# Kernel tuning notes

Hardware: AMD Instinct MI355X
Metric: run time of the kernel (lower is better)

The kernel has to match this reference:

```python
import jax, jax.numpy as jnp
import numpy as np

FEATURE_DIM = 256
NUM_HEADS = 8
HEAD_DIM = FEATURE_DIM // NUM_HEADS
LOCAL_RADIUS = 3.0
N_CUR = 4096
N_HIST = 4096
COORD_EXTENT = 16.0


def setup_inputs() -> dict:
    key = jax.random.key(0)
    ks = jax.random.split(key, 12)
    s = 1.0 / np.sqrt(FEATURE_DIM)  # ~nn.Linear init scale
    return {
        "current_feats": jax.random.normal(ks[0], (N_CUR, FEATURE_DIM), jnp.float32),
        "historical_feats": jax.random.normal(ks[1], (N_HIST, FEATURE_DIM), jnp.float32),
        "current_coords": jax.random.uniform(ks[2], (N_CUR, 3), jnp.float32) * COORD_EXTENT,
        "historical_coords": jax.random.uniform(ks[3], (N_HIST, 3), jnp.float32) * COORD_EXTENT,
        "Wq": jax.random.normal(ks[4], (FEATURE_DIM, FEATURE_DIM), jnp.float32) * s,
        "bq": jnp.zeros((FEATURE_DIM,), jnp.float32),
        "Wk": jax.random.normal(ks[5], (FEATURE_DIM, FEATURE_DIM), jnp.float32) * s,
        "bk": jnp.zeros((FEATURE_DIM,), jnp.float32),
        "Wv": jax.random.normal(ks[6], (FEATURE_DIM, FEATURE_DIM), jnp.float32) * s,
        "bv": jnp.zeros((FEATURE_DIM,), jnp.float32),
        "Wo": jax.random.normal(ks[7], (FEATURE_DIM, FEATURE_DIM), jnp.float32) * s,
        "bo": jnp.zeros((FEATURE_DIM,), jnp.float32),
    }


def reference(current_feats, historical_feats, current_coords, historical_coords,
              Wq, bq, Wk, bk, Wv, bv, Wo, bo):
    # local mask: squared distance <= radius^2 (identical to norm <= radius)
    diff = current_coords[:, None, :] - historical_coords[None, :, :]  # [Nq, Nk, 3]
    local_mask = jnp.sum(diff * diff, axis=-1) <= LOCAL_RADIUS ** 2      # [Nq, Nk]

    q = (current_feats @ Wq.T + bq).reshape(N_CUR, NUM_HEADS, HEAD_DIM)
    k = (historical_feats @ Wk.T + bk).reshape(N_HIST, NUM_HEADS, HEAD_DIM)
    v = (historical_feats @ Wv.T + bv).reshape(N_HIST, NUM_HEADS, HEAD_DIM)

    scores = jnp.einsum('qhd,khd->qhk', q, k) / np.sqrt(HEAD_DIM)        # [Nq, H, Nk]
    scores = jnp.where(local_mask[:, None, :], scores, -jnp.inf)
    attn = jax.nn.softmax(scores, axis=-1)  # dropout is identity in eval
    out = jnp.einsum('qhk,khd->qhd', attn, v).reshape(N_CUR, FEATURE_DIM)
    return out @ Wo.T + bo
```

## Files before the change

kernel.cpp:

```cpp
#include <hip/hip_runtime.h>
#include <math.h>

#define FDIM 256
#define NH 8
#define HD 32
#define NQ 4096
#define NKEY 4096
#define CAP 512
#define R2 9.0f

typedef _Float16 half8 __attribute__((ext_vector_type(8)));
typedef _Float16 half4v __attribute__((ext_vector_type(4)));
typedef float f32x4 __attribute__((ext_vector_type(4)));
typedef unsigned short ushort_t;

#define CB_CUR  0
#define CB_HIST 1048576
#define CB_WQ   2097152
#define CB_WK   2162688
#define CB_WV   2228224
#define CB_WO   2293760
#define CB_F4_TOTAL 589824

__global__ __launch_bounds__(256) void prep(const float* __restrict__ cur,
                                            const float* __restrict__ hist,
                                            const float* __restrict__ Wq,
                                            const float* __restrict__ Wk,
                                            const float* __restrict__ Wv,
                                            const float* __restrict__ Wo,
                                            _Float16* __restrict__ dst,
                                            const float* __restrict__ qc,
                                            const float* __restrict__ kc,
                                            ushort_t* __restrict__ nbr,
                                            int* __restrict__ cnt) {
    if (blockIdx.x < 1024) {
        const int q    = blockIdx.x * 4 + (threadIdx.x >> 6);
        const int lane = threadIdx.x & 63;
        const float qx = qc[q * 3 + 0];
        const float qy = qc[q * 3 + 1];
        const float qz = qc[q * 3 + 2];
        int base = 0;
        for (int k0 = 0; k0 < NKEY; k0 += 64) {
            const int k = k0 + lane;
            float dx = __fsub_rn(qx, kc[k * 3 + 0]);
            float dy = __fsub_rn(qy, kc[k * 3 + 1]);
            float dz = __fsub_rn(qz, kc[k * 3 + 2]);
            float d2 = __fadd_rn(__fadd_rn(__fmul_rn(dx, dx), __fmul_rn(dy, dy)),
                                 __fmul_rn(dz, dz));
            bool valid = (d2 <= R2);
            unsigned long long bal = __ballot(valid);
            if (valid) {
                int pos = base + __popcll(bal & ((1ull << lane) - 1ull));
                if (pos < CAP) nbr[(size_t)q * CAP + pos] = (ushort_t)k;
            }
            base += __popcll(bal);
        }
        if (lane == 0) cnt[q] = (base > CAP) ? CAP : base;
    } else {
        const int stride = 1024 * 256;
        for (int i4 = (blockIdx.x - 1024) * 256 + threadIdx.x; i4 < CB_F4_TOTAL;
             i4 += stride) {
            const float* src;
            int base;
            if (i4 < 262144)      { src = cur;  base = 0; }
            else if (i4 < 524288) { src = hist; base = 262144; }
            else if (i4 < 540672) { src = Wq;   base = 524288; }
            else if (i4 < 557056) { src = Wk;   base = 540672; }
            else if (i4 < 573440) { src = Wv;   base = 557056; }
            else                  { src = Wo;   base = 573440; }
            float4 v = ((const float4*)src)[i4 - base];
            half4v h;
            h[0] = (_Float16)v.x; h[1] = (_Float16)v.y;
            h[2] = (_Float16)v.z; h[3] = (_Float16)v.w;
            ((half4v*)dst)[i4] = h;
        }
    }
}

__device__ __forceinline__ void mfma_tile_16x64(const _Float16* __restrict__ A,
                                                const _Float16* __restrict__ W,
                                                int m0, int n0, int wave, int lane,
                                                f32x4 acc[4]) {
    const int row  = lane & 15;
    const int quad = lane >> 4;
    const _Float16* aptr = A + (size_t)(m0 + wave * 16 + row) * 256 + quad * 8;
    const _Float16* wptr = W + (size_t)(n0 + row) * 256 + quad * 8;
#pragma unroll
    for (int i = 0; i < 4; ++i) acc[i] = (f32x4){0.f, 0.f, 0.f, 0.f};
#pragma unroll
    for (int k0 = 0; k0 < 8; ++k0) {
        half8 a = *(const half8*)(aptr + k0 * 32);
#pragma unroll
        for (int nt = 0; nt < 4; ++nt) {
            half8 b = *(const half8*)(wptr + (size_t)nt * 16 * 256 + k0 * 32);
            acc[nt] = __builtin_amdgcn_mfma_f32_16x16x32_f16(a, b, acc[nt], 0, 0, 0);
        }
    }
}

__global__ __launch_bounds__(256) void qkv_mfma(const _Float16* __restrict__ cb,
                                                const float* __restrict__ bq,
                                                const float* __restrict__ bk,
                                                const float* __restrict__ bv,
                                                float* __restrict__ Qout,
                                                _Float16* __restrict__ KV) {
    const int z    = blockIdx.z;
    const int wave = threadIdx.x >> 6;
    const int lane = threadIdx.x & 63;
    const int m0   = blockIdx.y * 64;
    const int n0   = blockIdx.x * 64;

    const _Float16* A = (z == 0) ? (cb + CB_CUR) : (cb + CB_HIST);
    const _Float16* W = (z == 0) ? (cb + CB_WQ) : (z == 1) ? (cb + CB_WK) : (cb + CB_WV);
    const float* bias = (z == 0) ? bq : (z == 1) ? bk : bv;

    f32x4 acc[4];
    mfma_tile_16x64(A, W, m0, n0, wave, lane, acc);

    const int col  = lane & 15;
    const int quad = lane >> 4;
    float bs[4];
#pragma unroll
    for (int nt = 0; nt < 4; ++nt) bs[nt] = bias[n0 + nt * 16 + col];

    if (z == 0) {
#pragma unroll
        for (int nt = 0; nt < 4; ++nt)
#pragma unroll
            for (int r = 0; r < 4; ++r)
                Qout[(size_t)(m0 + wave * 16 + quad * 4 + r) * 256 + n0 + nt * 16 + col] =
                    acc[nt][r] + bs[nt];
    } else {
        const int off = (z == 1) ? 0 : 256;
#pragma unroll
        for (int nt = 0; nt < 4; ++nt)
#pragma unroll
            for (int r = 0; r < 4; ++r)
                KV[(size_t)(m0 + wave * 16 + quad * 4 + r) * 512 + off + n0 + nt * 16 + col] =
                    (_Float16)(acc[nt][r] + bs[nt]);
    }
}

__global__ __launch_bounds__(256) void o_mfma(const _Float16* __restrict__ Ob,
                                              const _Float16* __restrict__ Wo,
                                              const float* __restrict__ bo,
                                              float* __restrict__ out) {
    const int wave = threadIdx.x >> 6;
    const int lane = threadIdx.x & 63;
    const int m0   = blockIdx.y * 64;
    const int n0   = blockIdx.x * 64;

    f32x4 acc[4];
    mfma_tile_16x64(Ob, Wo, m0, n0, wave, lane, acc);

    const int col  = lane & 15;
    const int quad = lane >> 4;
#pragma unroll
    for (int nt = 0; nt < 4; ++nt) {
        const float b = bo[n0 + nt * 16 + col];
#pragma unroll
        for (int r = 0; r < 4; ++r)
            out[(size_t)(m0 + wave * 16 + quad * 4 + r) * 256 + n0 + nt * 16 + col] =
                acc[nt][r] + b;
    }
}

__global__ __launch_bounds__(256) void sparse_attn6(const float* __restrict__ Q,
                                                    const _Float16* __restrict__ KV,
                                                    const ushort_t* __restrict__ nbr,
                                                    const int* __restrict__ cnt,
                                                    _Float16* __restrict__ Ob) {
    __shared__ float sm[4][32][12];
    const int q    = blockIdx.x;
    const int t    = threadIdx.x;
    const int wave = t >> 6;
    const int lane = t & 63;
    const int p    = lane >> 5;
    const int h    = (lane >> 2) & 7;
    const int s    = lane & 3;

    float qv[8];
    {
        const float* qrow = Q + (size_t)q * FDIM + h * HD + s * 8;
        float4 a = ((const float4*)qrow)[0];
        float4 b = ((const float4*)qrow)[1];
        const float sc = 0.17677669529663687f;
        qv[0] = a.x * sc; qv[1] = a.y * sc; qv[2] = a.z * sc; qv[3] = a.w * sc;
        qv[4] = b.x * sc; qv[5] = b.y * sc; qv[6] = b.z * sc; qv[7] = b.w * sc;
    }

    float o[8];
#pragma unroll
    for (int i = 0; i < 8; ++i) o[i] = 0.f;
    float m = -3e38f, l = 0.f;

    const int n = cnt[q];
    const ushort_t* nl = nbr + (size_t)q * CAP;
    const int koff = h * HD + s * 8;

    for (int j = 2 * wave + p; j < n; j += 8) {
        const int k = nl[j];
        const _Float16* r = KV + ((size_t)k << 9) + koff;
        half8 k8 = *(const half8*)(r);
        half8 v8 = *(const half8*)(r + 256);

        float part = 0.f;
#pragma unroll
        for (int i = 0; i < 8; ++i)
            part = fmaf(qv[i], (float)k8[i], part);
        part += __shfl_xor(part, 1, 64);
        part += __shfl_xor(part, 2, 64);

        const float nm = fmaxf(m, part);
        const float sf = __expf(m - nm);
        const float pw = __expf(part - nm);
        l = l * sf + pw;
#pragma unroll
        for (int i = 0; i < 8; ++i)
            o[i] = o[i] * sf + pw * (float)v8[i];
        m = nm;
    }

    {
        const float m2 = __shfl_xor(m, 32, 64);
        const float l2 = __shfl_xor(l, 32, 64);
        const float nm = fmaxf(m, m2);
        const float a  = __expf(m - nm);
        const float b  = __expf(m2 - nm);
        l = l * a + l2 * b;
#pragma unroll
        for (int i = 0; i < 8; ++i) {
            const float o2 = __shfl_xor(o[i], 32, 64);
            o[i] = o[i] * a + o2 * b;
        }
        m = nm;
    }

    if (lane < 32) {
        float* dst = &sm[wave][lane][0];
        *(float4*)(dst)     = (float4){o[0], o[1], o[2], o[3]};
        *(float4*)(dst + 4) = (float4){o[4], o[5], o[6], o[7]};
        dst[8] = m; dst[9] = l;
    }
    __syncthreads();

    if (t < 32) {
        float4 x0 = *(const float4*)&sm[0][t][0];
        float4 x1 = *(const float4*)&sm[0][t][4];
        float O[8] = {x0.x, x0.y, x0.z, x0.w, x1.x, x1.y, x1.z, x1.w};
        float M = sm[0][t][8], L = sm[0][t][9];
#pragma unroll
        for (int w = 1; w < 4; ++w) {
            float4 y0 = *(const float4*)&sm[w][t][0];
            float4 y1 = *(const float4*)&sm[w][t][4];
            const float m2 = sm[w][t][8], l2 = sm[w][t][9];
            const float nm = fmaxf(M, m2);
            const float a  = __expf(M - nm);
            const float b  = __expf(m2 - nm);
            L = L * a + l2 * b;
            float y[8] = {y0.x, y0.y, y0.z, y0.w, y1.x, y1.y, y1.z, y1.w};
#pragma unroll
            for (int i = 0; i < 8; ++i) O[i] = O[i] * a + y[i] * b;
            M = nm;
        }
        const float inv = 1.0f / L;
        half8 ho;
#pragma unroll
        for (int i = 0; i < 8; ++i) ho[i] = (_Float16)(O[i] * inv);
        *(half8*)(Ob + (size_t)q * FDIM + t * 8) = ho;
    }
}

extern "C" void kernel_launch(void* const* d_in, const int* in_sizes, int n_in,
                              void* d_out, int out_size, void* d_ws, size_t ws_size,
                              hipStream_t stream) {
    const float* cur_feats   = (const float*)d_in[0];
    const float* hist_feats  = (const float*)d_in[1];
    const float* cur_coords  = (const float*)d_in[2];
    const float* hist_coords = (const float*)d_in[3];
    const float* bq = (const float*)d_in[5];
    const float* bk = (const float*)d_in[7];
    const float* bv = (const float*)d_in[9];
    const float* bo = (const float*)d_in[11];
    float* out = (float*)d_out;

    char* w = (char*)d_ws;
    float*     Qb   = (float*)(w);
    _Float16*  KV   = (_Float16*)(w + (4 << 20));
    ushort_t*  nbr  = (ushort_t*)(w + (8 << 20));
    int*       cnt  = (int*)(w + (12 << 20));
    _Float16*  Ob   = (_Float16*)(w + (12 << 20) + (64 << 10));
    _Float16*  cb   = (_Float16*)(w + (15 << 20));

    prep<<<2048, 256, 0, stream>>>(cur_feats, hist_feats,
                                   (const float*)d_in[4], (const float*)d_in[6],
                                   (const float*)d_in[8], (const float*)d_in[10], cb,
                                   cur_coords, hist_coords, nbr, cnt);

    qkv_mfma<<<dim3(4, 64, 3), 256, 0, stream>>>(cb, bq, bk, bv, Qb, KV);

    sparse_attn6<<<NQ, 256, 0, stream>>>(Qb, KV, nbr, cnt, Ob);

    o_mfma<<<dim3(4, 64), 256, 0, stream>>>(Ob, cb + CB_WO, bo, out);
}
```

Baseline: 150.1 us.

## Group spatially nearby queries per block to share K/V neighbor loads

Queries are binned into a 6x6x6 spatial grid, and each attention block handles up to four queries from the same cell. The block builds a shared union of their neighbor lists with per-query masks, so each K/V row is loaded once and used for all four queries. Q is also stored in fp16 to halve its traffic. In exchange the block pays bitmap and union-list construction with atomics and extra syncs, and does masked softmax work on keys outside a query's own radius.

After: 230.7 us. 53.7% more time.

```diff
diff --git a/kernel.cpp b/kernel.cpp
--- a/kernel.cpp
+++ b/kernel.cpp
@@ -8,6 +8,14 @@
 #define NKEY 4096
 #define CAP 512
 #define R2 9.0f
+
+#define NCELL 6
+#define NC3   216
+#define CCAP  64
+#define NGRP  16
+#define GBLK  (NC3 * NGRP)
+#define OCAP  512
+#define OBLK  64
 
 typedef _Float16 half8 __attribute__((ext_vector_type(8)));
 typedef _Float16 half4v __attribute__((ext_vector_type(4)));
@@ -32,7 +40,11 @@
                                             const float* __restrict__ qc,
                                             const float* __restrict__ kc,
                                             ushort_t* __restrict__ nbr,
-                                            int* __restrict__ cnt) {
+                                            int* __restrict__ cnt,
+                                            int* __restrict__ ccnt,
+                                            int* __restrict__ cellq,
+                                            int* __restrict__ ocnt,
+                                            int* __restrict__ oq) {
     if (blockIdx.x < 1024) {
         const int q    = blockIdx.x * 4 + (threadIdx.x >> 6);
         const int lane = threadIdx.x & 63;
@@ -56,7 +68,7 @@
             base += __popcll(bal);
         }
         if (lane == 0) cnt[q] = (base > CAP) ? CAP : base;
-    } else {
+    } else if (blockIdx.x < 2048) {
         const int stride = 1024 * 256;
         for (int i4 = (blockIdx.x - 1024) * 256 + threadIdx.x; i4 < CB_F4_TOTAL;
              i4 += stride) {
@@ -74,6 +86,19 @@
             h[2] = (_Float16)v.z; h[3] = (_Float16)v.w;
             ((half4v*)dst)[i4] = h;
         }
+    } else {
+        const int q = (blockIdx.x - 2048) * 256 + threadIdx.x;
+        const float s = (float)NCELL / 16.0f;
+        int ix = (int)(qc[q * 3 + 0] * s);
+        int iy = (int)(qc[q * 3 + 1] * s);
+        int iz = (int)(qc[q * 3 + 2] * s);
+        ix = min(NCELL - 1, max(0, ix));
+        iy = min(NCELL - 1, max(0, iy));
+        iz = min(NCELL - 1, max(0, iz));
+        const int cell = (iz * NCELL + iy) * NCELL + ix;
+        const int slot = atomicAdd(&ccnt[cell], 1);
+        if (slot < CCAP) cellq[cell * CCAP + slot] = q;
+        else { int o = atomicAdd(ocnt, 1); if (o < OCAP) oq[o] = q; }
     }
 }
 
@@ -102,7 +127,7 @@
                                                 const float* __restrict__ bq,
                                                 const float* __restrict__ bk,
                                                 const float* __restrict__ bv,
-                                                float* __restrict__ Qout,
+                                                _Float16* __restrict__ Qh,
                                                 _Float16* __restrict__ KV) {
     const int z    = blockIdx.z;
     const int wave = threadIdx.x >> 6;
@@ -128,8 +153,8 @@
         for (int nt = 0; nt < 4; ++nt)
 #pragma unroll
             for (int r = 0; r < 4; ++r)
-                Qout[(size_t)(m0 + wave * 16 + quad * 4 + r) * 256 + n0 + nt * 16 + col] =
-                    acc[nt][r] + bs[nt];
+                Qh[(size_t)(m0 + wave * 16 + quad * 4 + r) * 256 + n0 + nt * 16 + col] =
+                    (_Float16)(acc[nt][r] + bs[nt]);
     } else {
         const int off = (z == 1) ? 0 : 256;
 #pragma unroll
@@ -165,109 +190,203 @@
     }
 }
 
-__global__ __launch_bounds__(256) void sparse_attn6(const float* __restrict__ Q,
-                                                    const _Float16* __restrict__ KV,
-                                                    const ushort_t* __restrict__ nbr,
-                                                    const int* __restrict__ cnt,
-                                                    _Float16* __restrict__ Ob) {
-    __shared__ float sm[4][32][12];
-    const int q    = blockIdx.x;
-    const int t    = threadIdx.x;
-    const int wave = t >> 6;
-    const int lane = t & 63;
-    const int p    = lane >> 5;
-    const int h    = (lane >> 2) & 7;
-    const int s    = lane & 3;
-
-    float qv[8];
+__device__ __forceinline__ void process_group(
+        int q0, int q1, int q2, int q3, int nq,
+        const _Float16* __restrict__ Qh, const _Float16* __restrict__ KV,
+        const ushort_t* __restrict__ nbr, const int* __restrict__ cnt,
+        _Float16* __restrict__ Ob,
+        unsigned int (*bm)[128], unsigned int* ulist, int* ucnt,
+        float (*sm)[32][40], int wave, int lane) {
+    const int t  = threadIdx.x;
+    const int p  = lane >> 5;
+    const int hs = lane & 31;
+    const int qids[4] = {q0, q1, q2, q3};
+
+    if (t < 128) { bm[0][t] = 0; bm[1][t] = 0; bm[2][t] = 0; bm[3][t] = 0; }
+    if (t == 0) *ucnt = 0;
+    __syncthreads();
+
+    if (wave < nq) {
+        const int qw = qids[wave];
+        const int nw = cnt[qw];
+        const ushort_t* nl = nbr + (size_t)qw * CAP;
+        for (int j = lane; j < nw; j += 64) {
+            const int k = nl[j];
+            atomicOr(&bm[wave][k >> 5], 1u << (k & 31));
+        }
+    }
+    __syncthreads();
+
+    if (t < 128) {
+        const unsigned int b0 = bm[0][t], b1 = bm[1][t];
+        const unsigned int b2 = bm[2][t], b3 = bm[3][t];
+        unsigned int u = b0 | b1 | b2 | b3;
+        const int c = __popc(u);
+        int pos = c ? atomicAdd(ucnt, c) : 0;
+        while (u) {
+            const int b = __ffs(u) - 1;
+            u &= u - 1;
+            const unsigned int msk = ((b0 >> b) & 1u) | (((b1 >> b) & 1u) << 1) |
+                                     (((b2 >> b) & 1u) << 2) | (((b3 >> b) & 1u) << 3);
+            ulist[pos++] = (unsigned int)(t * 32 + b) | (msk << 16);
+        }
+    }
+    __syncthreads();
+    const int U = *ucnt;
+
+    float qv[4][8];
     {
-        const float* qrow = Q + (size_t)q * FDIM + h * HD + s * 8;
-        float4 a = ((const float4*)qrow)[0];
-        float4 b = ((const float4*)qrow)[1];
         const float sc = 0.17677669529663687f;
-        qv[0] = a.x * sc; qv[1] = a.y * sc; qv[2] = a.z * sc; qv[3] = a.w * sc;
-        qv[4] = b.x * sc; qv[5] = b.y * sc; qv[6] = b.z * sc; qv[7] = b.w * sc;
-    }
-
-    float o[8];
-#pragma unroll
-    for (int i = 0; i < 8; ++i) o[i] = 0.f;
-    float m = -3e38f, l = 0.f;
-
-    const int n = cnt[q];
-    const ushort_t* nl = nbr + (size_t)q * CAP;
-    const int koff = h * HD + s * 8;
-
-    for (int j = 2 * wave + p; j < n; j += 8) {
-        const int k = nl[j];
-        const _Float16* r = KV + ((size_t)k << 9) + koff;
+#pragma unroll
+        for (int w = 0; w < 4; ++w) {
+            half8 qh = *(const half8*)(Qh + (size_t)qids[w] * FDIM + hs * 8);
+#pragma unroll
+            for (int i = 0; i < 8; ++i) qv[w][i] = (float)qh[i] * sc;
+        }
+    }
+
+    float o[4][8];
+#pragma unroll
+    for (int w = 0; w < 4; ++w)
+#pragma unroll
+        for (int i = 0; i < 8; ++i) o[w][i] = 0.f;
+    float mm[4] = {-3e38f, -3e38f, -3e38f, -3e38f};
+    float ll[4] = {0.f, 0.f, 0.f, 0.f};
+
+    const int hw = wave * 2 + p;
+    for (int j = hw; j < U; j += 8) {
+        const unsigned int e   = ulist[j];
+        const int          k   = e & 0xFFFF;
+        const unsigned int msk = e >> 16;
+        const _Float16* r = KV + ((size_t)k << 9) + hs * 8;
         half8 k8 = *(const half8*)(r);
         half8 v8 = *(const half8*)(r + 256);
 
-        float part = 0.f;
-#pragma unroll
-        for (int i = 0; i < 8; ++i)
-            part = fmaf(qv[i], (float)k8[i], part);
-        part += __shfl_xor(part, 1, 64);
-        part += __shfl_xor(part, 2, 64);
-
-        const float nm = fmaxf(m, part);
-        const float sf = __expf(m - nm);
-        const float pw = __expf(part - nm);
-        l = l * sf + pw;
-#pragma unroll
-        for (int i = 0; i < 8; ++i)
-            o[i] = o[i] * sf + pw * (float)v8[i];
-        m = nm;
-    }
-
-    {
-        const float m2 = __shfl_xor(m, 32, 64);
-        const float l2 = __shfl_xor(l, 32, 64);
-        const float nm = fmaxf(m, m2);
-        const float a  = __expf(m - nm);
+        float dd[4] = {0.f, 0.f, 0.f, 0.f};
+#pragma unroll
+        for (int i = 0; i < 8; ++i) {
+            const float kf = (float)k8[i];
+            dd[0] = fmaf(qv[0][i], kf, dd[0]);
+            dd[1] = fmaf(qv[1][i], kf, dd[1]);
+            dd[2] = fmaf(qv[2][i], kf, dd[2]);
+            dd[3] = fmaf(qv[3][i], kf, dd[3]);
+        }
+#pragma unroll
+        for (int w = 0; w < 4; ++w) {
+            dd[w] += __shfl_xor(dd[w], 1, 64);
+            dd[w] += __shfl_xor(dd[w], 2, 64);
+        }
+        float vf[8];
+#pragma unroll
+        for (int i = 0; i < 8; ++i) vf[i] = (float)v8[i];
+
+#pragma unroll
+        for (int w = 0; w < 4; ++w) {
+            const float sc = ((msk >> w) & 1u) ? dd[w] : -INFINITY;
+            const float nm = fmaxf(mm[w], sc);
+            const float sf = __expf(mm[w] - nm);
+            const float pw = __expf(sc - nm);
+            ll[w] = ll[w] * sf + pw;
+#pragma unroll
+            for (int i = 0; i < 8; ++i)
+                o[w][i] = o[w][i] * sf + pw * vf[i];
+            mm[w] = nm;
+        }
+    }
+
+#pragma unroll
+    for (int w = 0; w < 4; ++w) {
+        const float m2 = __shfl_xor(mm[w], 32, 64);
+        const float l2 = __shfl_xor(ll[w], 32, 64);
+        const float nm = fmaxf(mm[w], m2);
+        const float a  = __expf(mm[w] - nm);
         const float b  = __expf(m2 - nm);
-        l = l * a + l2 * b;
+        ll[w] = ll[w] * a + l2 * b;
 #pragma unroll
         for (int i = 0; i < 8; ++i) {
-            const float o2 = __shfl_xor(o[i], 32, 64);
-            o[i] = o[i] * a + o2 * b;
-        }
-        m = nm;
+            const float o2 = __shfl_xor(o[w][i], 32, 64);
+            o[w][i] = o[w][i] * a + o2 * b;
+        }
+        mm[w] = nm;
     }
 
     if (lane < 32) {
-        float* dst = &sm[wave][lane][0];
-        *(float4*)(dst)     = (float4){o[0], o[1], o[2], o[3]};
-        *(float4*)(dst + 4) = (float4){o[4], o[5], o[6], o[7]};
-        dst[8] = m; dst[9] = l;
+        float* d = &sm[wave][lane][0];
+#pragma unroll
+        for (int w = 0; w < 4; ++w) {
+#pragma unroll
+            for (int i = 0; i < 8; ++i) d[w * 10 + i] = o[w][i];
+            d[w * 10 + 8] = mm[w];
+            d[w * 10 + 9] = ll[w];
+        }
     }
     __syncthreads();
 
     if (t < 32) {
-        float4 x0 = *(const float4*)&sm[0][t][0];
-        float4 x1 = *(const float4*)&sm[0][t][4];
-        float O[8] = {x0.x, x0.y, x0.z, x0.w, x1.x, x1.y, x1.z, x1.w};
-        float M = sm[0][t][8], L = sm[0][t][9];
-#pragma unroll
-        for (int w = 1; w < 4; ++w) {
-            float4 y0 = *(const float4*)&sm[w][t][0];
-            float4 y1 = *(const float4*)&sm[w][t][4];
-            const float m2 = sm[w][t][8], l2 = sm[w][t][9];
-            const float nm = fmaxf(M, m2);
-            const float a  = __expf(M - nm);
-            const float b  = __expf(m2 - nm);
-            L = L * a + l2 * b;
-            float y[8] = {y0.x, y0.y, y0.z, y0.w, y1.x, y1.y, y1.z, y1.w};
-#pragma unroll
-            for (int i = 0; i < 8; ++i) O[i] = O[i] * a + y[i] * b;
-            M = nm;
-        }
-        const float inv = 1.0f / L;
-        half8 ho;
-#pragma unroll
-        for (int i = 0; i < 8; ++i) ho[i] = (_Float16)(O[i] * inv);
-        *(half8*)(Ob + (size_t)q * FDIM + t * 8) = ho;
+        for (int w = 0; w < nq; ++w) {
+            float O[8], M, L;
+            {
+                const float* d = &sm[0][t][w * 10];
+#pragma unroll
+                for (int i = 0; i < 8; ++i) O[i] = d[i];
+                M = d[8]; L = d[9];
+            }
+#pragma unroll
+            for (int wv = 1; wv < 4; ++wv) {
+                const float* d = &sm[wv][t][w * 10];
+                const float m2 = d[8], l2 = d[9];
+                const float nm = fmaxf(M, m2);
+                const float a  = __expf(M - nm);
+                const float b  = __expf(m2 - nm);
+                L = L * a + l2 * b;
+#pragma unroll
+                for (int i = 0; i < 8; ++i) O[i] = O[i] * a + d[i] * b;
+                M = nm;
+            }
+            const float inv = 1.0f / L;
+            half8 ho;
+#pragma unroll
+            for (int i = 0; i < 8; ++i) ho[i] = (_Float16)(O[i] * inv);
+            *(half8*)(Ob + (size_t)qids[w] * FDIM + t * 8) = ho;
+        }
+    }
+    __syncthreads();
+}
+
+__global__ __launch_bounds__(256) void sparse_attn8(
+        const _Float16* __restrict__ Qh, const _Float16* __restrict__ KV,
+        const ushort_t* __restrict__ nbr, const int* __restrict__ cnt,
+        const int* __restrict__ ccnt, const int* __restrict__ cellq,
+        const int* __restrict__ ocnt, const int* __restrict__ oq,
+        _Float16* __restrict__ Ob) {
+    __shared__ unsigned int bm[4][128];
+    __shared__ unsigned int ulist[2048];
+    __shared__ int ucnt;
+    __shared__ float sm[4][32][40];
+    const int wave = threadIdx.x >> 6;
+    const int lane = threadIdx.x & 63;
+
+    if (blockIdx.x < GBLK) {
+        const int c    = blockIdx.x >> 4;
+        const int g    = blockIdx.x & 15;
+        const int cc   = min(ccnt[c], CCAP);
+        const int base = g * 4;
+        if (base >= cc) return;
+        const int nq = min(4, cc - base);
+        const int* cb = cellq + c * CCAP + base;
+        const int q0 = cb[0];
+        const int q1 = cb[(nq > 1) ? 1 : 0];
+        const int q2 = cb[(nq > 2) ? 2 : 0];
+        const int q3 = cb[(nq > 3) ? 3 : 0];
+        process_group(q0, q1, q2, q3, nq, Qh, KV, nbr, cnt, Ob,
+                      bm, ulist, &ucnt, sm, wave, lane);
+    } else {
+        const int oc = min(*ocnt, OCAP);
+        for (int i = blockIdx.x - GBLK; i < oc; i += OBLK) {
+            const int qq = oq[i];
+            process_group(qq, qq, qq, qq, 1, Qh, KV, nbr, cnt, Ob,
+                          bm, ulist, &ucnt, sm, wave, lane);
+        }
     }
 }
 
@@ -285,21 +404,29 @@
     float* out = (float*)d_out;
 
     char* w = (char*)d_ws;
-    float*     Qb   = (float*)(w);
+    _Float16*  Qh   = (_Float16*)(w);
     _Float16*  KV   = (_Float16*)(w + (4 << 20));
     ushort_t*  nbr  = (ushort_t*)(w + (8 << 20));
     int*       cnt  = (int*)(w + (12 << 20));
     _Float16*  Ob   = (_Float16*)(w + (12 << 20) + (64 << 10));
     _Float16*  cb   = (_Float16*)(w + (15 << 20));
-
-    prep<<<2048, 256, 0, stream>>>(cur_feats, hist_feats,
+    int*       ccnt = (int*)(w + (20 << 20));
+    int*       ocnt = ccnt + NC3;
+    int*       cellq= (int*)(w + (20 << 20) + 1024);
+    int*       oq   = (int*)(w + (20 << 20) + 1024 + NC3 * CCAP * 4);
+
+    hipMemsetAsync(ccnt, 0, (NC3 + 1) * sizeof(int), stream);
+
+    prep<<<2064, 256, 0, stream>>>(cur_feats, hist_feats,
                                    (const float*)d_in[4], (const float*)d_in[6],
                                    (const float*)d_in[8], (const float*)d_in[10], cb,
-                                   cur_coords, hist_coords, nbr, cnt);
-
-    qkv_mfma<<<dim3(4, 64, 3), 256, 0, stream>>>(cb, bq, bk, bv, Qb, KV);
-
-    sparse_attn6<<<NQ, 256, 0, stream>>>(Qb, KV, nbr, cnt, Ob);
+                                   cur_coords, hist_coords, nbr, cnt,
+                                   ccnt, cellq, ocnt, oq);
+
+    qkv_mfma<<<dim3(4, 64, 3), 256, 0, stream>>>(cb, bq, bk, bv, Qh, KV);
+
+    sparse_attn8<<<GBLK + OBLK, 256, 0, stream>>>(Qh, KV, nbr, cnt,
+                                                  ccnt, cellq, ocnt, oq, Ob);
 
     o_mfma<<<dim3(4, 64), 256, 0, stream>>>(Ob, cb + CB_WO, bo, out);
 }
```
